# Kernel optimization log

Measured on AMD Instinct MI355X. Metric: run time of the kernel, lower is better.

## Reference

```python
import jax, jax.numpy as jnp
import numpy as np

N_NODES = 50000
N_EDGES = 1000000
N_QUERY = 100000
NUM_FEATURES = 256
HIDDEN = 256
LABEL_DIM = 2


def glorot(key, shape):
    lim = float(np.sqrt(6.0 / (shape[0] + shape[1])))
    return jax.random.uniform(key, shape, jnp.float32, -lim, lim)


def setup_inputs() -> dict:
    key = jax.random.key(0)
    ks = jax.random.split(key, 8)
    x = jax.random.normal(ks[0], (N_NODES, NUM_FEATURES), jnp.float32)
    edge_index = jax.random.randint(ks[1], (2, N_EDGES), 0, N_NODES)
    query_edges = jax.random.randint(ks[2], (N_QUERY, 2), 0, N_NODES)
    edge_weight = jax.random.uniform(ks[3], (N_EDGES,), jnp.float32)
    W1 = glorot(ks[4], (NUM_FEATURES, HIDDEN))
    b1 = jnp.zeros((HIDDEN,), jnp.float32)
    W2 = glorot(ks[5], (HIDDEN, HIDDEN))
    b2 = jnp.zeros((HIDDEN,), jnp.float32)
    Wl = glorot(ks[6], (2 * HIDDEN, LABEL_DIM))
    bl = jnp.zeros((LABEL_DIM,), jnp.float32)
    return {"x": x, "edge_index": edge_index, "query_edges": query_edges,
            "edge_weight": edge_weight, "W1": W1, "b1": b1, "W2": W2,
            "b2": b2, "Wl": Wl, "bl": bl}


def digcn_conv(x, edge_index, edge_weight, W, b):
    # x: [N, F_in] -> h: [N, F_out]; propagate: out[dst] += w_e * h[src]
    h = x @ W
    src, dst = edge_index[0], edge_index[1]
    msg = h[src] * edge_weight[:, None]            # [E, F_out]
    agg = jax.ops.segment_sum(msg, dst, num_segments=x.shape[0])
    return agg + b


def reference(x, edge_index, query_edges, edge_weight, W1, b1, W2, b2, Wl, bl):
    h = jax.nn.relu(digcn_conv(x, edge_index, edge_weight, W1, b1))
    # dropout is identity at eval time
    h = digcn_conv(h, edge_index, edge_weight, W2, b2)
    q = jnp.concatenate((h[query_edges[:, 0]], h[query_edges[:, 1]]), axis=-1)
    logits = q @ Wl + bl
    return jax.nn.log_softmax(logits, axis=1)
```

## Files before the change

kernel.cpp:

```cpp
#include <hip/hip_runtime.h>
#include <hip/hip_bf16.h>
#include <math.h>

typedef __bf16 bf16;
typedef __bf16 v8bf __attribute__((ext_vector_type(8)));
typedef __bf16 v4bf __attribute__((ext_vector_type(4)));
typedef float  v4f  __attribute__((ext_vector_type(4)));

#define FDIM 256
#define BKT_CAP 8192
#define AROW 264
#define P3CAP 4096


__global__ __launch_bounds__(256) void flag_kernel(float* __restrict__ out, int n) {
  int i = blockIdx.x * 256 + threadIdx.x;
  if (i < n) out[i] = 1.0e9f;
}

__global__ __launch_bounds__(256) void k1_prep(const float* __restrict__ W1,
                                               const float* __restrict__ W2,
                                               bf16* __restrict__ Wt1,
                                               const int* __restrict__ dst,
                                               int* __restrict__ phist,
                                               const float* __restrict__ Wl,
                                               const float* __restrict__ b2,
                                               const float* __restrict__ bl,
                                               float4* __restrict__ V,
                                               float* __restrict__ cc,
                                               int E, int N, int nbkt) {
  __shared__ int h[256];
  __shared__ float sWl[1024];
  __shared__ float red[256];
  int b = blockIdx.x;
  int t = threadIdx.x;
  if (b < 256) {
    int k = b;
    Wt1[t * FDIM + k] = (bf16)W1[k * FDIM + t];
  } else if (b < 512) {
    int pb = b - 256;
    int chunk = (E + 255) >> 8;
    int lo = pb * chunk;
    int hi = lo + chunk; if (hi > E) hi = E;
    h[t] = 0;
    __syncthreads();
    for (int e = lo + t; e < hi; e += 256) {
      int d = dst[e];
      d = d < 0 ? 0 : (d >= N ? N - 1 : d);
      atomicAdd(&h[d >> 8], 1);
    }
    __syncthreads();
    phist[pb * 256 + t] = h[t];
  } else {
#pragma unroll
    for (int j = 0; j < 4; ++j) sWl[j * 256 + t] = Wl[j * 256 + t];
    __syncthreads();
    const float* w2row = W2 + (size_t)t * FDIM;
    float4 acc = make_float4(0.f, 0.f, 0.f, 0.f);
    for (int j = 0; j < 256; ++j) {
      float w = w2row[j];
      acc.x += w * sWl[2 * j + 0];
      acc.y += w * sWl[2 * j + 1];
      acc.z += w * sWl[512 + 2 * j + 0];
      acc.w += w * sWl[512 + 2 * j + 1];
    }
    V[t] = acc;
    float bj = b2[t];
    red[t] = bj * (sWl[2 * t + 0] + sWl[512 + 2 * t + 0]);
    __syncthreads();
    if (t == 0) {
      float s = 0.f;
      for (int j = 0; j < 256; ++j) s += red[j];
      cc[0] = s + bl[0];
    }
    __syncthreads();
    red[t] = bj * (sWl[2 * t + 1] + sWl[512 + 2 * t + 1]);
    __syncthreads();
    if (t == 0) {
      float s = 0.f;
      for (int j = 0; j < 256; ++j) s += red[j];
      cc[1] = s + bl[1];
    }
  }
}

__global__ __launch_bounds__(256) void p2_scan(const int* __restrict__ phist,
                                               int* __restrict__ bbase,
                                               int* __restrict__ pbase,
                                               int* __restrict__ offs,
                                               int nbkt, int Nn) {
  __shared__ int wsum[4];
  int t = threadIdx.x, lane = t & 63, wv = t >> 6;
  int v = 0;
  for (int pb = 0; pb < 256; ++pb) v += phist[pb * 256 + t];
  if (t >= nbkt) v = 0;
  int x = v;
#pragma unroll
  for (int d = 1; d < 64; d <<= 1) {
    int y = __shfl_up(x, d, 64);
    if (lane >= d) x += y;
  }
  if (lane == 63) wsum[wv] = x;
  __syncthreads();
  int woff = 0;
  if (wv >= 1) woff += wsum[0];
  if (wv >= 2) woff += wsum[1];
  if (wv >= 3) woff += wsum[2];
  int incl = woff + x;
  int excl = incl - v;
  if (t < nbkt) bbase[t] = excl;
  if (t == 255) {
    bbase[nbkt] = incl;
    offs[Nn] = incl;
  }
  int run = excl;
#pragma unroll 4
  for (int pb = 0; pb < 256; ++pb) {
    pbase[pb * 256 + t] = run;
    run += phist[pb * 256 + t];
  }
}

__device__ inline void stage64(const float* __restrict__ A, bf16* __restrict__ As,
                               int row0, int M, int tid) {
#pragma unroll
  for (int j = 0; j < 8; ++j) {
    int g = j * 2048 + tid * 8;
    int r = g >> 8, c = g & 255;
    int gr = row0 + r; if (gr >= M) gr = M - 1;
    const float* p = A + (size_t)gr * FDIM + c;
    float4 f0 = *reinterpret_cast<const float4*>(p);
    float4 f1 = *reinterpret_cast<const float4*>(p + 4);
    v8bf o;
    o[0] = (bf16)f0.x; o[1] = (bf16)f0.y; o[2] = (bf16)f0.z; o[3] = (bf16)f0.w;
    o[4] = (bf16)f1.x; o[5] = (bf16)f1.y; o[6] = (bf16)f1.z; o[7] = (bf16)f1.w;
    *reinterpret_cast<v8bf*>(As + r * AROW + c) = o;
  }
}

__global__ __launch_bounds__(256, 2) void gemm1(const float* __restrict__ A,
                                                const bf16* __restrict__ Bt,
                                                bf16* __restrict__ C, int M) {
  __shared__ bf16 As[64 * AROW];
  const int K = FDIM, N = FDIM;
  int tid = threadIdx.x;
  int wave = tid >> 6;
  int lane = tid & 63;
  int l15 = lane & 15, quad = lane >> 4;

  v8bf bfr[4][8];
#pragma unroll
  for (int nn = 0; nn < 4; ++nn) {
    const bf16* bp = Bt + (size_t)(wave * 64 + nn * 16 + l15) * K + quad * 8;
#pragma unroll
    for (int kk = 0; kk < 8; ++kk)
      bfr[nn][kk] = *reinterpret_cast<const v8bf*>(bp + kk * 32);
  }

  int ntiles = (M + 63) >> 6;
  for (int tile = blockIdx.x; tile < ntiles; tile += gridDim.x) {
    int row0 = tile * 64;
    __syncthreads();
    stage64(A, As, row0, M, tid);
    __syncthreads();

#pragma unroll
    for (int st = 0; st < 4; ++st) {
      v8bf afr[8];
#pragma unroll
      for (int kk = 0; kk < 8; ++kk)
        afr[kk] = *reinterpret_cast<const v8bf*>(As + (st * 16 + l15) * AROW + quad * 8 + kk * 32);

      v4f acc[4];
#pragma unroll
      for (int nn = 0; nn < 4; ++nn) acc[nn] = (v4f){0.f, 0.f, 0.f, 0.f};

#pragma unroll
      for (int kk = 0; kk < 8; ++kk)
#pragma unroll
        for (int nn = 0; nn < 4; ++nn)
          acc[nn] = __builtin_amdgcn_mfma_f32_16x16x32_bf16(afr[kk], bfr[nn][kk], acc[nn], 0, 0, 0);

#pragma unroll
      for (int nn = 0; nn < 4; ++nn)
#pragma unroll
        for (int r = 0; r < 4; ++r) {
          int row = row0 + st * 16 + quad * 4 + r;
          int col = wave * 64 + nn * 16 + l15;
          if (row < M) C[(size_t)row * N + col] = (bf16)acc[nn][r];
        }
    }
  }
}

__global__ __launch_bounds__(256) void p3_scatter(const int* __restrict__ src,
                                                  const int* __restrict__ dst,
                                                  const float* __restrict__ ew,
                                                  const int* __restrict__ phist,
                                                  const int* __restrict__ pbase,
                                                  uint2* __restrict__ tmp,
                                                  int E, int N) {
  __shared__ uint2 ent[P3CAP];
  __shared__ int lbase[256];
  __shared__ int lcnt[256];
  __shared__ int gbase[256];
  __shared__ int wsum[4];
  int pb = blockIdx.x, t = threadIdx.x, lane = t & 63, wv = t >> 6;
  int chunk = (E + 255) >> 8;
  int lo = pb * chunk;
  int hi = lo + chunk; if (hi > E) hi = E;

  int v = phist[pb * 256 + t];
  int x = v;
#pragma unroll
  for (int d = 1; d < 64; d <<= 1) {
    int y = __shfl_up(x, d, 64);
    if (lane >= d) x += y;
  }
  if (lane == 63) wsum[wv] = x;
  gbase[t] = pbase[pb * 256 + t];
  lcnt[t] = 0;
  __syncthreads();
  int woff = 0;
  if (wv >= 1) woff += wsum[0];
  if (wv >= 2) woff += wsum[1];
  if (wv >= 3) woff += wsum[2];
  lbase[t] = woff + x - v;
  __syncthreads();

  for (int e = lo + t; e < hi; e += 256) {
    int d = dst[e];
    d = d < 0 ? 0 : (d >= N ? N - 1 : d);
    int b = d >> 8;
    int sv = src[e];
    sv = sv < 0 ? 0 : (sv >= N ? N - 1 : sv);
    unsigned int u = __float_as_uint(ew[e]);
    unsigned int wbits = ((u + 0x7FFFu + ((u >> 16) & 1u)) & 0xFFFF0000u);
    unsigned int meta = wbits | (unsigned int)(sv & 0xFFFF);
    int r = atomicAdd(&lcnt[b], 1);
    int pos = lbase[b] + r;
    if (pos >= 0 && pos < P3CAP) ent[pos] = make_uint2(meta, (unsigned int)d);
  }
  __syncthreads();

  int count = hi - lo;
  for (int i = t; i < count; i += 256) {
    uint2 en = ent[i];
    int b = (int)(en.y >> 8);
    int dest = gbase[b] + (i - lbase[b]);
    if (dest >= 0 && dest < E) tmp[dest] = en;
  }
}

__global__ __launch_bounds__(256, 1) void p4_sort(const uint2* __restrict__ tmp,
                                                  const int* __restrict__ bbase,
                                                  unsigned int* __restrict__ pmeta,
                                                  int* __restrict__ offs,
                                                  int Nn, int E) {
  __shared__ uint2 ent[BKT_CAP];
  __shared__ unsigned int outm[BKT_CAP];
  __shared__ int h2[256], ex2[256], c2[256];
  __shared__ int wsum[4];
  int b = blockIdx.x, t = threadIdx.x, lane = t & 63, wv = t >> 6;
  int s0 = bbase[b], s1 = bbase[b + 1];
  int count = s1 - s0;
  if (count < 0) count = 0;
  if (count > BKT_CAP) count = BKT_CAP;
  for (int i = t; i < count; i += 256) ent[i] = tmp[s0 + i];
  h2[t] = 0; c2[t] = 0;
  __syncthreads();
  for (int i = t; i < count; i += 256) atomicAdd(&h2[ent[i].y & 255u], 1);
  __syncthreads();
  int v = h2[t];
  int x = v;
#pragma unroll
  for (int d = 1; d < 64; d <<= 1) {
    int y = __shfl_up(x, d, 64);
    if (lane >= d) x += y;
  }
  if (lane == 63) wsum[wv] = x;
  __syncthreads();
  int woff = 0;
  if (wv >= 1) woff += wsum[0];
  if (wv >= 2) woff += wsum[1];
  if (wv >= 3) woff += wsum[2];
  int excl = woff + x - v;
  ex2[t] = excl;
  int node = (b << 8) + t;
  if (node < Nn) offs[node] = s0 + excl;
  __syncthreads();
  for (int i = t; i < count; i += 256) {
    int l = (int)(ent[i].y & 255u);
    int r = atomicAdd(&c2[l], 1);
    outm[ex2[l] + r] = ent[i].x;
  }
  __syncthreads();
  for (int i = t; i < count; i += 256) pmeta[s0 + i] = outm[i];
}

__global__ __launch_bounds__(256) void agg1G(const bf16* __restrict__ T,
                                             const unsigned int* __restrict__ pmeta,
                                             const int* __restrict__ offsets,
                                             const float* __restrict__ bias,
                                             const float4* __restrict__ V,
                                             float4* __restrict__ G,
                                             int node_lo, int node_hi, int E, int N) {
  int wid = blockIdx.x * 4 + (threadIdx.x >> 6);
  int nw = gridDim.x * 4;
  int lane = threadIdx.x & 63;
  int f = lane * 4;
  const bf16* Tf = T + f;

  float4 bb = *reinterpret_cast<const float4*>(bias + f);
  float4 v0 = V[f + 0], v1 = V[f + 1], v2 = V[f + 2], v3 = V[f + 3];

  for (int node = node_lo + wid; node < node_hi; node += nw) {
    int nb = __builtin_amdgcn_readfirstlane(node);
    int beg = offsets[nb], end = offsets[nb + 1];
    beg = beg < 0 ? 0 : (beg > E ? E : beg);
    end = end < beg ? beg : (end > E ? E : end);
    int cnt = end - beg;
    const unsigned int* m = pmeta + beg;

    float a0 = 0.f, a1 = 0.f, a2 = 0.f, a3 = 0.f;
    int p = 0;
    for (; p + 8 <= cnt; p += 8) {
      unsigned int mv0 = m[p + 0], mv1 = m[p + 1], mv2 = m[p + 2], mv3 = m[p + 3];
      unsigned int mv4 = m[p + 4], mv5 = m[p + 5], mv6 = m[p + 6], mv7 = m[p + 7];
      v4bf t0 = *reinterpret_cast<const v4bf*>(Tf + ((size_t)(mv0 & 0xFFFFu) << 8));
      v4bf t1 = *reinterpret_cast<const v4bf*>(Tf + ((size_t)(mv1 & 0xFFFFu) << 8));
      v4bf t2 = *reinterpret_cast<const v4bf*>(Tf + ((size_t)(mv2 & 0xFFFFu) << 8));
      v4bf t3 = *reinterpret_cast<const v4bf*>(Tf + ((size_t)(mv3 & 0xFFFFu) << 8));
      v4bf t4 = *reinterpret_cast<const v4bf*>(Tf + ((size_t)(mv4 & 0xFFFFu) << 8));
      v4bf t5 = *reinterpret_cast<const v4bf*>(Tf + ((size_t)(mv5 & 0xFFFFu) << 8));
      v4bf t6 = *reinterpret_cast<const v4bf*>(Tf + ((size_t)(mv6 & 0xFFFFu) << 8));
      v4bf t7 = *reinterpret_cast<const v4bf*>(Tf + ((size_t)(mv7 & 0xFFFFu) << 8));
      float w0 = __uint_as_float(mv0 & 0xFFFF0000u);
      float w1 = __uint_as_float(mv1 & 0xFFFF0000u);
      float w2 = __uint_as_float(mv2 & 0xFFFF0000u);
      float w3 = __uint_as_float(mv3 & 0xFFFF0000u);
      float w4 = __uint_as_float(mv4 & 0xFFFF0000u);
      float w5 = __uint_as_float(mv5 & 0xFFFF0000u);
      float w6 = __uint_as_float(mv6 & 0xFFFF0000u);
      float w7 = __uint_as_float(mv7 & 0xFFFF0000u);
      a0 += w0 * (float)t0[0]; a1 += w0 * (float)t0[1]; a2 += w0 * (float)t0[2]; a3 += w0 * (float)t0[3];
      a0 += w1 * (float)t1[0]; a1 += w1 * (float)t1[1]; a2 += w1 * (float)t1[2]; a3 += w1 * (float)t1[3];
      a0 += w2 * (float)t2[0]; a1 += w2 * (float)t2[1]; a2 += w2 * (float)t2[2]; a3 += w2 * (float)t2[3];
      a0 += w3 * (float)t3[0]; a1 += w3 * (float)t3[1]; a2 += w3 * (float)t3[2]; a3 += w3 * (float)t3[3];
      a0 += w4 * (float)t4[0]; a1 += w4 * (float)t4[1]; a2 += w4 * (float)t4[2]; a3 += w4 * (float)t4[3];
      a0 += w5 * (float)t5[0]; a1 += w5 * (float)t5[1]; a2 += w5 * (float)t5[2]; a3 += w5 * (float)t5[3];
      a0 += w6 * (float)t6[0]; a1 += w6 * (float)t6[1]; a2 += w6 * (float)t6[2]; a3 += w6 * (float)t6[3];
      a0 += w7 * (float)t7[0]; a1 += w7 * (float)t7[1]; a2 += w7 * (float)t7[2]; a3 += w7 * (float)t7[3];
    }
    for (; p < cnt; ++p) {
      unsigned int mv = m[p];
      float w = __uint_as_float(mv & 0xFFFF0000u);
      v4bf tv = *reinterpret_cast<const v4bf*>(Tf + ((size_t)(mv & 0xFFFFu) << 8));
      a0 += w * (float)tv[0];
      a1 += w * (float)tv[1];
      a2 += w * (float)tv[2];
      a3 += w * (float)tv[3];
    }

    float r0 = fmaxf(a0 + bb.x, 0.f);
    float r1 = fmaxf(a1 + bb.y, 0.f);
    float r2 = fmaxf(a2 + bb.z, 0.f);
    float r3 = fmaxf(a3 + bb.w, 0.f);

    float gx = r0 * v0.x + r1 * v1.x + r2 * v2.x + r3 * v3.x;
    float gy = r0 * v0.y + r1 * v1.y + r2 * v2.y + r3 * v3.y;
    float gz = r0 * v0.z + r1 * v1.z + r2 * v2.z + r3 * v3.z;
    float gw = r0 * v0.w + r1 * v1.w + r2 * v2.w + r3 * v3.w;
#pragma unroll
    for (int d = 32; d > 0; d >>= 1) {
      gx += __shfl_down(gx, d, 64);
      gy += __shfl_down(gy, d, 64);
      gz += __shfl_down(gz, d, 64);
      gw += __shfl_down(gw, d, 64);
    }
    if (lane == 0) G[node] = make_float4(gx, gy, gz, gw);
  }
}

__global__ __launch_bounds__(256) void aggP(const float4* __restrict__ G,
                                            const unsigned int* __restrict__ pmeta,
                                            const int* __restrict__ offsets,
                                            float4* __restrict__ P, int N, int E) {
  int node = blockIdx.x * 64 + (threadIdx.x >> 2);
  if (node >= N) return;
  int j = threadIdx.x & 3;
  int beg = offsets[node], end = offsets[node + 1];
  beg = beg < 0 ? 0 : (beg > E ? E : beg);
  end = end < beg ? beg : (end > E ? E : end);
  float ax = 0.f, ay = 0.f, az = 0.f, aw = 0.f;
  int p = beg + j;
  for (; p + 4 < end; p += 8) {
    unsigned int m0 = pmeta[p], m1 = pmeta[p + 4];
    int s0 = (int)(m0 & 0xFFFFu); s0 = s0 >= N ? N - 1 : s0;
    int s1 = (int)(m1 & 0xFFFFu); s1 = s1 >= N ? N - 1 : s1;
    float4 g0 = G[s0], g1 = G[s1];
    float w0 = __uint_as_float(m0 & 0xFFFF0000u);
    float w1 = __uint_as_float(m1 & 0xFFFF0000u);
    ax += w0 * g0.x + w1 * g1.x;
    ay += w0 * g0.y + w1 * g1.y;
    az += w0 * g0.z + w1 * g1.z;
    aw += w0 * g0.w + w1 * g1.w;
  }
  if (p < end) {
    unsigned int mm = pmeta[p];
    int s = (int)(mm & 0xFFFFu); s = s >= N ? N - 1 : s;
    float w = __uint_as_float(mm & 0xFFFF0000u);
    float4 g = G[s];
    ax += w * g.x; ay += w * g.y; az += w * g.z; aw += w * g.w;
  }
  ax += __shfl_xor(ax, 1, 64); ax += __shfl_xor(ax, 2, 64);
  ay += __shfl_xor(ay, 1, 64); ay += __shfl_xor(ay, 2, 64);
  az += __shfl_xor(az, 1, 64); az += __shfl_xor(az, 2, 64);
  aw += __shfl_xor(aw, 1, 64); aw += __shfl_xor(aw, 2, 64);
  if (j == 0) P[node] = make_float4(ax, ay, az, aw);
}

__global__ __launch_bounds__(256) void query_small(const int* __restrict__ qe,
                                                   const float4* __restrict__ P,
                                                   const float* __restrict__ cc,
                                                   float* __restrict__ out, int Q, int N) {
  int q = blockIdx.x * 256 + threadIdx.x;
  if (q >= Q) return;
  int n0 = qe[2 * q + 0]; n0 = n0 < 0 ? 0 : (n0 >= N ? N - 1 : n0);
  int n1 = qe[2 * q + 1]; n1 = n1 < 0 ? 0 : (n1 >= N ? N - 1 : n1);
  float4 p0 = P[n0];
  float4 p1 = P[n1];
  float l0 = p0.x + p1.z + cc[0];
  float l1 = p0.y + p1.w + cc[1];
  float m = fmaxf(l0, l1);
  float lse = m + logf(expf(l0 - m) + expf(l1 - m));
  out[2 * q + 0] = l0 - lse;
  out[2 * q + 1] = l1 - lse;
}


extern "C" void kernel_launch(void* const* d_in, const int* in_sizes, int n_in,
                              void* d_out, int out_size, void* d_ws, size_t ws_size,
                              hipStream_t stream) {
  const float* x  = (const float*)d_in[0];
  const int*   ei = (const int*)d_in[1];
  const int*   qe = (const int*)d_in[2];
  const float* ew = (const float*)d_in[3];
  const float* W1 = (const float*)d_in[4];
  const float* b1 = (const float*)d_in[5];
  const float* W2 = (const float*)d_in[6];
  const float* b2 = (const float*)d_in[7];
  const float* Wl = (const float*)d_in[8];
  const float* bl = (const float*)d_in[9];

  int N = in_sizes[0] / FDIM;
  int E = in_sizes[1] / 2;
  int Q = in_sizes[2] / 2;
  const int* srcv = ei;
  const int* dstv = ei + E;
  int nbkt = (N + 255) >> 8;
  int ntiles = (N + 63) >> 6;

  size_t off = 0;
  auto alloc = [&](size_t bytes) -> void* {
    void* p = (char*)d_ws + off;
    off += (bytes + 255) & ~(size_t)255;
    return p;
  };
  bf16* bufT  = (bf16*)alloc((size_t)N * FDIM * 2);
  uint2* tmp  = (uint2*)alloc((size_t)E * 8);
  bf16* Wt1   = (bf16*)alloc((size_t)FDIM * FDIM * 2);
  int* offs   = (int*)alloc((size_t)(N + 1) * 4);
  unsigned int* pmeta = (unsigned int*)alloc((size_t)E * 4);
  float4* G   = (float4*)alloc((size_t)N * 16);
  float4* P   = (float4*)alloc((size_t)N * 16);
  float4* V   = (float4*)alloc(256 * 16);
  float* cc   = (float*)alloc(2 * 4);
  int* phist  = (int*)alloc(256 * 256 * 4);
  int* pbase  = (int*)alloc(256 * 256 * 4);
  int* bbase  = (int*)alloc(257 * 4);

  if (off > ws_size) {
    flag_kernel<<<(out_size + 255) / 256, 256, 0, stream>>>((float*)d_out, out_size);
    return;
  }

  k1_prep<<<513, 256, 0, stream>>>(W1, W2, Wt1, dstv, phist, Wl, b2, bl, V, cc,
                                   E, N, nbkt);
  p2_scan<<<1, 256, 0, stream>>>(phist, bbase, pbase, offs, nbkt, N);
  gemm1<<<ntiles, 256, 0, stream>>>(x, Wt1, bufT, N);
  p3_scatter<<<256, 256, 0, stream>>>(srcv, dstv, ew, phist, pbase, tmp, E, N);
  p4_sort<<<nbkt, 256, 0, stream>>>(tmp, bbase, pmeta, offs, N, E);

  int q1 = N >> 2, q2 = N >> 1, q3 = q1 + q2;
  agg1G<<<2048, 256, 0, stream>>>(bufT, pmeta, offs, b1, V, G, 0, q1, E, N);
  agg1G<<<2048, 256, 0, stream>>>(bufT, pmeta, offs, b1, V, G, q1, q2, E, N);
  agg1G<<<2048, 256, 0, stream>>>(bufT, pmeta, offs, b1, V, G, q2, q3, E, N);
  agg1G<<<2048, 256, 0, stream>>>(bufT, pmeta, offs, b1, V, G, q3, N, E, N);

  aggP<<<(N * 4 + 255) / 256, 256, 0, stream>>>(G, pmeta, offs, P, N, E);

  query_small<<<(Q + 255) / 256, 256, 0, stream>>>(qe, P, cc, (float*)d_out, Q, N);
}
```

Baseline: 279.5 us.

## Fold global bucket scan into scatter/sort kernels and merge agg1G launches

Removes the single-block p2_scan kernel by having each p3_scatter and p4_sort block recompute the column-sum and prefix scan of the partition histogram redundantly. It also replaces four quarter-range agg1G launches with one launch over all nodes. The goal is fewer kernel launches and less serialization on a tiny one-block kernel. The cost is that every block now reads the full 256x256 histogram, which adds redundant global loads.

```diff
diff --git a/kernel.cpp b/kernel.cpp
--- a/kernel.cpp
+++ b/kernel.cpp
@@ -84,43 +84,6 @@
   }
 }
 
-__global__ __launch_bounds__(256) void p2_scan(const int* __restrict__ phist,
-                                               int* __restrict__ bbase,
-                                               int* __restrict__ pbase,
-                                               int* __restrict__ offs,
-                                               int nbkt, int Nn) {
-  __shared__ int wsum[4];
-  int t = threadIdx.x, lane = t & 63, wv = t >> 6;
-  int v = 0;
-  for (int pb = 0; pb < 256; ++pb) v += phist[pb * 256 + t];
-  if (t >= nbkt) v = 0;
-  int x = v;
-#pragma unroll
-  for (int d = 1; d < 64; d <<= 1) {
-    int y = __shfl_up(x, d, 64);
-    if (lane >= d) x += y;
-  }
-  if (lane == 63) wsum[wv] = x;
-  __syncthreads();
-  int woff = 0;
-  if (wv >= 1) woff += wsum[0];
-  if (wv >= 2) woff += wsum[1];
-  if (wv >= 3) woff += wsum[2];
-  int incl = woff + x;
-  int excl = incl - v;
-  if (t < nbkt) bbase[t] = excl;
-  if (t == 255) {
-    bbase[nbkt] = incl;
-    offs[Nn] = incl;
-  }
-  int run = excl;
-#pragma unroll 4
-  for (int pb = 0; pb < 256; ++pb) {
-    pbase[pb * 256 + t] = run;
-    run += phist[pb * 256 + t];
-  }
-}
-
 __device__ inline void stage64(const float* __restrict__ A, bf16* __restrict__ As,
                                int row0, int M, int tid) {
 #pragma unroll
@@ -197,7 +160,6 @@
                                                   const int* __restrict__ dst,
                                                   const float* __restrict__ ew,
                                                   const int* __restrict__ phist,
-                                                  const int* __restrict__ pbase,
                                                   uint2* __restrict__ tmp,
                                                   int E, int N) {
   __shared__ uint2 ent[P3CAP];
@@ -210,22 +172,40 @@
   int lo = pb * chunk;
   int hi = lo + chunk; if (hi > E) hi = E;
 
-  int v = phist[pb * 256 + t];
-  int x = v;
+  int tot = 0, pref = 0, mine = 0;
+  for (int c = 0; c < 256; ++c) {
+    int v = phist[c * 256 + t];
+    if (c == pb) { pref = tot; mine = v; }
+    tot += v;
+  }
+  int x = tot;
 #pragma unroll
   for (int d = 1; d < 64; d <<= 1) {
     int y = __shfl_up(x, d, 64);
     if (lane >= d) x += y;
   }
   if (lane == 63) wsum[wv] = x;
-  gbase[t] = pbase[pb * 256 + t];
   lcnt[t] = 0;
   __syncthreads();
   int woff = 0;
   if (wv >= 1) woff += wsum[0];
   if (wv >= 2) woff += wsum[1];
   if (wv >= 3) woff += wsum[2];
-  lbase[t] = woff + x - v;
+  gbase[t] = (woff + x - tot) + pref;
+  __syncthreads();
+  int x2 = mine;
+#pragma unroll
+  for (int d = 1; d < 64; d <<= 1) {
+    int y = __shfl_up(x2, d, 64);
+    if (lane >= d) x2 += y;
+  }
+  if (lane == 63) wsum[wv] = x2;
+  __syncthreads();
+  int woff2 = 0;
+  if (wv >= 1) woff2 += wsum[0];
+  if (wv >= 2) woff2 += wsum[1];
+  if (wv >= 3) woff2 += wsum[2];
+  lbase[t] = woff2 + x2 - mine;
   __syncthreads();
 
   for (int e = lo + t; e < hi; e += 256) {
@@ -253,38 +233,60 @@
 }
 
 __global__ __launch_bounds__(256, 1) void p4_sort(const uint2* __restrict__ tmp,
-                                                  const int* __restrict__ bbase,
+                                                  const int* __restrict__ phist,
                                                   unsigned int* __restrict__ pmeta,
                                                   int* __restrict__ offs,
                                                   int Nn, int E) {
   __shared__ uint2 ent[BKT_CAP];
   __shared__ unsigned int outm[BKT_CAP];
   __shared__ int h2[256], ex2[256], c2[256];
+  __shared__ int exb[256], totb[256];
   __shared__ int wsum[4];
   int b = blockIdx.x, t = threadIdx.x, lane = t & 63, wv = t >> 6;
-  int s0 = bbase[b], s1 = bbase[b + 1];
+
+  int tot = 0;
+  for (int c = 0; c < 256; ++c) tot += phist[c * 256 + t];
+  int x = tot;
+#pragma unroll
+  for (int d = 1; d < 64; d <<= 1) {
+    int y = __shfl_up(x, d, 64);
+    if (lane >= d) x += y;
+  }
+  if (lane == 63) wsum[wv] = x;
+  h2[t] = 0; c2[t] = 0;
+  __syncthreads();
+  int woff = 0;
+  if (wv >= 1) woff += wsum[0];
+  if (wv >= 2) woff += wsum[1];
+  if (wv >= 3) woff += wsum[2];
+  exb[t] = woff + x - tot;
+  totb[t] = tot;
+  __syncthreads();
+  int s0 = exb[b];
+  int s1 = s0 + totb[b];
+  if (b == 0 && t == 0) offs[Nn] = exb[255] + totb[255];
+
   int count = s1 - s0;
   if (count < 0) count = 0;
   if (count > BKT_CAP) count = BKT_CAP;
   for (int i = t; i < count; i += 256) ent[i] = tmp[s0 + i];
-  h2[t] = 0; c2[t] = 0;
   __syncthreads();
   for (int i = t; i < count; i += 256) atomicAdd(&h2[ent[i].y & 255u], 1);
   __syncthreads();
   int v = h2[t];
-  int x = v;
+  int x2 = v;
 #pragma unroll
   for (int d = 1; d < 64; d <<= 1) {
-    int y = __shfl_up(x, d, 64);
-    if (lane >= d) x += y;
-  }
-  if (lane == 63) wsum[wv] = x;
-  __syncthreads();
-  int woff = 0;
-  if (wv >= 1) woff += wsum[0];
-  if (wv >= 2) woff += wsum[1];
-  if (wv >= 3) woff += wsum[2];
-  int excl = woff + x - v;
+    int y = __shfl_up(x2, d, 64);
+    if (lane >= d) x2 += y;
+  }
+  if (lane == 63) wsum[wv] = x2;
+  __syncthreads();
+  int woff2 = 0;
+  if (wv >= 1) woff2 += wsum[0];
+  if (wv >= 2) woff2 += wsum[1];
+  if (wv >= 3) woff2 += wsum[2];
+  int excl = woff2 + x2 - v;
   ex2[t] = excl;
   int node = (b << 8) + t;
   if (node < Nn) offs[node] = s0 + excl;
@@ -303,8 +305,7 @@
                                              const int* __restrict__ offsets,
                                              const float* __restrict__ bias,
                                              const float4* __restrict__ V,
-                                             float4* __restrict__ G,
-                                             int node_lo, int node_hi, int E, int N) {
+                                             float4* __restrict__ G, int N, int E) {
   int wid = blockIdx.x * 4 + (threadIdx.x >> 6);
   int nw = gridDim.x * 4;
   int lane = threadIdx.x & 63;
@@ -314,7 +315,7 @@
   float4 bb = *reinterpret_cast<const float4*>(bias + f);
   float4 v0 = V[f + 0], v1 = V[f + 1], v2 = V[f + 2], v3 = V[f + 3];
 
-  for (int node = node_lo + wid; node < node_hi; node += nw) {
+  for (int node = wid; node < N; node += nw) {
     int nb = __builtin_amdgcn_readfirstlane(node);
     int beg = offsets[nb], end = offsets[nb + 1];
     beg = beg < 0 ? 0 : (beg > E ? E : beg);
@@ -477,8 +478,6 @@
   float4* V   = (float4*)alloc(256 * 16);
   float* cc   = (float*)alloc(2 * 4);
   int* phist  = (int*)alloc(256 * 256 * 4);
-  int* pbase  = (int*)alloc(256 * 256 * 4);
-  int* bbase  = (int*)alloc(257 * 4);
 
   if (off > ws_size) {
     flag_kernel<<<(out_size + 255) / 256, 256, 0, stream>>>((float*)d_out, out_size);
@@ -487,16 +486,11 @@
 
   k1_prep<<<513, 256, 0, stream>>>(W1, W2, Wt1, dstv, phist, Wl, b2, bl, V, cc,
                                    E, N, nbkt);
-  p2_scan<<<1, 256, 0, stream>>>(phist, bbase, pbase, offs, nbkt, N);
   gemm1<<<ntiles, 256, 0, stream>>>(x, Wt1, bufT, N);
-  p3_scatter<<<256, 256, 0, stream>>>(srcv, dstv, ew, phist, pbase, tmp, E, N);
-  p4_sort<<<nbkt, 256, 0, stream>>>(tmp, bbase, pmeta, offs, N, E);
-
-  int q1 = N >> 2, q2 = N >> 1, q3 = q1 + q2;
-  agg1G<<<2048, 256, 0, stream>>>(bufT, pmeta, offs, b1, V, G, 0, q1, E, N);
-  agg1G<<<2048, 256, 0, stream>>>(bufT, pmeta, offs, b1, V, G, q1, q2, E, N);
-  agg1G<<<2048, 256, 0, stream>>>(bufT, pmeta, offs, b1, V, G, q2, q3, E, N);
-  agg1G<<<2048, 256, 0, stream>>>(bufT, pmeta, offs, b1, V, G, q3, N, E, N);
+  p3_scatter<<<256, 256, 0, stream>>>(srcv, dstv, ew, phist, tmp, E, N);
+  p4_sort<<<nbkt, 256, 0, stream>>>(tmp, phist, pmeta, offs, N, E);
+
+  agg1G<<<2048, 256, 0, stream>>>(bufT, pmeta, offs, b1, V, G, N, E);
 
   aggP<<<(N * 4 + 255) / 256, 256, 0, stream>>>(G, pmeta, offs, P, N, E);
 
```

Result: faster. 261.9 us (-6.3%).

## Fuse pipeline stages into two cooperative persistent kernels with grid syncs

Applied to the files above, without the earlier changes.

Collapses the chain of small launches (prep, scan, GEMM, scatter, sort, four aggregation passes, projection, query) into two cooperative kernels that separate phases with grid.sync(), removing launch overhead and inter-kernel gaps. The p4 sort now writes to global memory directly instead of staging through a shared output buffer, which lowers its shared memory use. The fallback path also merges the four split aggregation launches into one. In exchange, megaA runs with a fixed grid of 512 blocks, so the GEMM and sort get fewer blocks than before and are limited by the shared-memory occupancy of the fused kernel. If the cooperative launch fails, the code falls back to separate launches.

```diff
diff --git a/kernel.cpp b/kernel.cpp
--- a/kernel.cpp
+++ b/kernel.cpp
@@ -1,6 +1,9 @@
 #include <hip/hip_runtime.h>
+#include <hip/hip_cooperative_groups.h>
 #include <hip/hip_bf16.h>
 #include <math.h>
+
+namespace cg = cooperative_groups;
 
 typedef __bf16 bf16;
 typedef __bf16 v8bf __attribute__((ext_vector_type(8)));
@@ -11,6 +14,7 @@
 #define BKT_CAP 8192
 #define AROW 264
 #define P3CAP 4096
+#define SMEM_A 68640
 
 
 __global__ __launch_bounds__(256) void flag_kernel(float* __restrict__ out, int n) {
@@ -18,27 +22,21 @@
   if (i < n) out[i] = 1.0e9f;
 }
 
-__global__ __launch_bounds__(256) void k1_prep(const float* __restrict__ W1,
-                                               const float* __restrict__ W2,
-                                               bf16* __restrict__ Wt1,
-                                               const int* __restrict__ dst,
-                                               int* __restrict__ phist,
-                                               const float* __restrict__ Wl,
-                                               const float* __restrict__ b2,
-                                               const float* __restrict__ bl,
-                                               float4* __restrict__ V,
-                                               float* __restrict__ cc,
-                                               int E, int N, int nbkt) {
-  __shared__ int h[256];
-  __shared__ float sWl[1024];
-  __shared__ float red[256];
-  int b = blockIdx.x;
+
+__device__ void k1_body(int vb, char* sm, const float* __restrict__ W1,
+                        const float* __restrict__ W2, bf16* __restrict__ Wt1,
+                        const int* __restrict__ dst, int* __restrict__ phist,
+                        const float* __restrict__ Wl, const float* __restrict__ b2,
+                        const float* __restrict__ bl, float4* __restrict__ V,
+                        float* __restrict__ cc, int E, int N) {
+  int* h = (int*)sm;
+  float* sWl = (float*)(sm + 1024);
+  float* red = (float*)(sm + 5120);
   int t = threadIdx.x;
-  if (b < 256) {
-    int k = b;
-    Wt1[t * FDIM + k] = (bf16)W1[k * FDIM + t];
-  } else if (b < 512) {
-    int pb = b - 256;
+  if (vb < 256) {
+    Wt1[t * FDIM + vb] = (bf16)W1[vb * FDIM + t];
+  } else if (vb < 512) {
+    int pb = vb - 256;
     int chunk = (E + 255) >> 8;
     int lo = pb * chunk;
     int hi = lo + chunk; if (hi > E) hi = E;
@@ -51,6 +49,7 @@
     }
     __syncthreads();
     phist[pb * 256 + t] = h[t];
+    __syncthreads();
   } else {
 #pragma unroll
     for (int j = 0; j < 4; ++j) sWl[j * 256 + t] = Wl[j * 256 + t];
@@ -81,15 +80,14 @@
       for (int j = 0; j < 256; ++j) s += red[j];
       cc[1] = s + bl[1];
     }
-  }
-}
-
-__global__ __launch_bounds__(256) void p2_scan(const int* __restrict__ phist,
-                                               int* __restrict__ bbase,
-                                               int* __restrict__ pbase,
-                                               int* __restrict__ offs,
-                                               int nbkt, int Nn) {
-  __shared__ int wsum[4];
+    __syncthreads();
+  }
+}
+
+__device__ void p2_body(char* sm, const int* __restrict__ phist,
+                        int* __restrict__ bbase, int* __restrict__ pbase,
+                        int* __restrict__ offs, int nbkt, int Nn) {
+  int* wsum = (int*)sm;
   int t = threadIdx.x, lane = t & 63, wv = t >> 6;
   int v = 0;
   for (int pb = 0; pb < 256; ++pb) v += phist[pb * 256 + t];
@@ -121,8 +119,8 @@
   }
 }
 
-__device__ inline void stage64(const float* __restrict__ A, bf16* __restrict__ As,
-                               int row0, int M, int tid) {
+__device__ void stage64(const float* __restrict__ A, bf16* __restrict__ As,
+                        int row0, int M, int tid) {
 #pragma unroll
   for (int j = 0; j < 8; ++j) {
     int g = j * 2048 + tid * 8;
@@ -138,10 +136,9 @@
   }
 }
 
-__global__ __launch_bounds__(256, 2) void gemm1(const float* __restrict__ A,
-                                                const bf16* __restrict__ Bt,
-                                                bf16* __restrict__ C, int M) {
-  __shared__ bf16 As[64 * AROW];
+__device__ void gemm_body(const float* __restrict__ A, const bf16* __restrict__ Bt,
+                          bf16* __restrict__ C, int M, int bid, int nblocks,
+                          bf16* As) {
   const int K = FDIM, N = FDIM;
   int tid = threadIdx.x;
   int wave = tid >> 6;
@@ -158,7 +155,7 @@
   }
 
   int ntiles = (M + 63) >> 6;
-  for (int tile = blockIdx.x; tile < ntiles; tile += gridDim.x) {
+  for (int tile = bid; tile < ntiles; tile += nblocks) {
     int row0 = tile * 64;
     __syncthreads();
     stage64(A, As, row0, M, tid);
@@ -193,19 +190,16 @@
   }
 }
 
-__global__ __launch_bounds__(256) void p3_scatter(const int* __restrict__ src,
-                                                  const int* __restrict__ dst,
-                                                  const float* __restrict__ ew,
-                                                  const int* __restrict__ phist,
-                                                  const int* __restrict__ pbase,
-                                                  uint2* __restrict__ tmp,
-                                                  int E, int N) {
-  __shared__ uint2 ent[P3CAP];
-  __shared__ int lbase[256];
-  __shared__ int lcnt[256];
-  __shared__ int gbase[256];
-  __shared__ int wsum[4];
-  int pb = blockIdx.x, t = threadIdx.x, lane = t & 63, wv = t >> 6;
+__device__ void p3_body(int pb, char* sm, const int* __restrict__ src,
+                        const int* __restrict__ dst, const float* __restrict__ ew,
+                        const int* __restrict__ phist, const int* __restrict__ pbase,
+                        uint2* __restrict__ tmp, int E, int N) {
+  uint2* ent = (uint2*)sm;
+  int* lbase = (int*)(sm + 32768);
+  int* lcnt  = (int*)(sm + 33792);
+  int* gbase = (int*)(sm + 34816);
+  int* wsum  = (int*)(sm + 35840);
+  int t = threadIdx.x, lane = t & 63, wv = t >> 6;
   int chunk = (E + 255) >> 8;
   int lo = pb * chunk;
   int hi = lo + chunk; if (hi > E) hi = E;
@@ -250,18 +244,18 @@
     int dest = gbase[b] + (i - lbase[b]);
     if (dest >= 0 && dest < E) tmp[dest] = en;
   }
-}
-
-__global__ __launch_bounds__(256, 1) void p4_sort(const uint2* __restrict__ tmp,
-                                                  const int* __restrict__ bbase,
-                                                  unsigned int* __restrict__ pmeta,
-                                                  int* __restrict__ offs,
-                                                  int Nn, int E) {
-  __shared__ uint2 ent[BKT_CAP];
-  __shared__ unsigned int outm[BKT_CAP];
-  __shared__ int h2[256], ex2[256], c2[256];
-  __shared__ int wsum[4];
-  int b = blockIdx.x, t = threadIdx.x, lane = t & 63, wv = t >> 6;
+  __syncthreads();
+}
+
+__device__ void p4_body(int b, char* sm, const uint2* __restrict__ tmp,
+                        const int* __restrict__ bbase, unsigned int* __restrict__ pmeta,
+                        int* __restrict__ offs, int Nn, int E) {
+  uint2* ent = (uint2*)sm;
+  int* h2  = (int*)(sm + 65536);
+  int* ex2 = (int*)(sm + 66560);
+  int* c2  = (int*)(sm + 67584);
+  int* wsum = (int*)(sm + 68608);
+  int t = threadIdx.x, lane = t & 63, wv = t >> 6;
   int s0 = bbase[b], s1 = bbase[b + 1];
   int count = s1 - s0;
   if (count < 0) count = 0;
@@ -292,19 +286,16 @@
   for (int i = t; i < count; i += 256) {
     int l = (int)(ent[i].y & 255u);
     int r = atomicAdd(&c2[l], 1);
-    outm[ex2[l] + r] = ent[i].x;
-  }
-  __syncthreads();
-  for (int i = t; i < count; i += 256) pmeta[s0 + i] = outm[i];
-}
-
-__global__ __launch_bounds__(256) void agg1G(const bf16* __restrict__ T,
-                                             const unsigned int* __restrict__ pmeta,
-                                             const int* __restrict__ offsets,
-                                             const float* __restrict__ bias,
-                                             const float4* __restrict__ V,
-                                             float4* __restrict__ G,
-                                             int node_lo, int node_hi, int E, int N) {
+    int pos = s0 + ex2[l] + r;
+    if (pos >= 0 && pos < E) pmeta[pos] = ent[i].x;
+  }
+  __syncthreads();
+}
+
+__device__ void agg_body(const bf16* __restrict__ T, const unsigned int* __restrict__ pmeta,
+                         const int* __restrict__ offsets, const float* __restrict__ bias,
+                         const float4* __restrict__ V, float4* __restrict__ G,
+                         int N, int E) {
   int wid = blockIdx.x * 4 + (threadIdx.x >> 6);
   int nw = gridDim.x * 4;
   int lane = threadIdx.x & 63;
@@ -314,7 +305,7 @@
   float4 bb = *reinterpret_cast<const float4*>(bias + f);
   float4 v0 = V[f + 0], v1 = V[f + 1], v2 = V[f + 2], v3 = V[f + 3];
 
-  for (int node = node_lo + wid; node < node_hi; node += nw) {
+  for (int node = wid; node < N; node += nw) {
     int nb = __builtin_amdgcn_readfirstlane(node);
     int beg = offsets[nb], end = offsets[nb + 1];
     beg = beg < 0 ? 0 : (beg > E ? E : beg);
@@ -382,60 +373,162 @@
   }
 }
 
+__device__ void aggP_body(const float4* __restrict__ G, const unsigned int* __restrict__ pmeta,
+                          const int* __restrict__ offsets, float4* __restrict__ P,
+                          int N, int E) {
+  int nvb = (N + 63) >> 6;
+  int j = threadIdx.x & 3;
+  for (int vb = blockIdx.x; vb < nvb; vb += gridDim.x) {
+    int node = vb * 64 + (threadIdx.x >> 2);
+    if (node < N) {
+      int beg = offsets[node], end = offsets[node + 1];
+      beg = beg < 0 ? 0 : (beg > E ? E : beg);
+      end = end < beg ? beg : (end > E ? E : end);
+      float ax = 0.f, ay = 0.f, az = 0.f, aw = 0.f;
+      int p = beg + j;
+      for (; p + 4 < end; p += 8) {
+        unsigned int m0 = pmeta[p], m1 = pmeta[p + 4];
+        int s0 = (int)(m0 & 0xFFFFu); s0 = s0 >= N ? N - 1 : s0;
+        int s1 = (int)(m1 & 0xFFFFu); s1 = s1 >= N ? N - 1 : s1;
+        float4 g0 = G[s0], g1 = G[s1];
+        float w0 = __uint_as_float(m0 & 0xFFFF0000u);
+        float w1 = __uint_as_float(m1 & 0xFFFF0000u);
+        ax += w0 * g0.x + w1 * g1.x;
+        ay += w0 * g0.y + w1 * g1.y;
+        az += w0 * g0.z + w1 * g1.z;
+        aw += w0 * g0.w + w1 * g1.w;
+      }
+      if (p < end) {
+        unsigned int mm = pmeta[p];
+        int s = (int)(mm & 0xFFFFu); s = s >= N ? N - 1 : s;
+        float w = __uint_as_float(mm & 0xFFFF0000u);
+        float4 g = G[s];
+        ax += w * g.x; ay += w * g.y; az += w * g.z; aw += w * g.w;
+      }
+      ax += __shfl_xor(ax, 1, 64); ax += __shfl_xor(ax, 2, 64);
+      ay += __shfl_xor(ay, 1, 64); ay += __shfl_xor(ay, 2, 64);
+      az += __shfl_xor(az, 1, 64); az += __shfl_xor(az, 2, 64);
+      aw += __shfl_xor(aw, 1, 64); aw += __shfl_xor(aw, 2, 64);
+      if (j == 0) P[node] = make_float4(ax, ay, az, aw);
+    }
+  }
+}
+
+__device__ void query_body(const int* __restrict__ qe, const float4* __restrict__ P,
+                           const float* __restrict__ cc, float* __restrict__ out,
+                           int Q, int N) {
+  int nvb = (Q + 255) >> 8;
+  for (int vb = blockIdx.x; vb < nvb; vb += gridDim.x) {
+    int q = vb * 256 + threadIdx.x;
+    if (q < Q) {
+      int n0 = qe[2 * q + 0]; n0 = n0 < 0 ? 0 : (n0 >= N ? N - 1 : n0);
+      int n1 = qe[2 * q + 1]; n1 = n1 < 0 ? 0 : (n1 >= N ? N - 1 : n1);
+      float4 p0 = P[n0];
+      float4 p1 = P[n1];
+      float l0 = p0.x + p1.z + cc[0];
+      float l1 = p0.y + p1.w + cc[1];
+      float m = fmaxf(l0, l1);
+      float lse = m + logf(expf(l0 - m) + expf(l1 - m));
+      out[2 * q + 0] = l0 - lse;
+      out[2 * q + 1] = l1 - lse;
+    }
+  }
+}
+
+
+__global__ __launch_bounds__(256, 2) void megaA(const float* __restrict__ W1,
+    const float* __restrict__ W2, bf16* __restrict__ Wt1, const int* __restrict__ dst,
+    int* __restrict__ phist, const float* __restrict__ Wl, const float* __restrict__ b2,
+    const float* __restrict__ bl, float4* __restrict__ V, float* __restrict__ cc,
+    int* __restrict__ bbase, int* __restrict__ pbase, int* __restrict__ offs,
+    const float* __restrict__ x, bf16* __restrict__ bufT, const int* __restrict__ src,
+    const float* __restrict__ ew, uint2* __restrict__ tmp,
+    unsigned int* __restrict__ pmeta, int E, int N, int nbkt) {
+  cg::grid_group grid = cg::this_grid();
+  __shared__ __align__(16) char sm[SMEM_A];
+
+  for (int vb = blockIdx.x; vb < 513; vb += gridDim.x)
+    k1_body(vb, sm, W1, W2, Wt1, dst, phist, Wl, b2, bl, V, cc, E, N);
+  grid.sync();
+  if (blockIdx.x == 0) p2_body(sm, phist, bbase, pbase, offs, nbkt, N);
+  grid.sync();
+  gemm_body(x, Wt1, bufT, N, blockIdx.x, gridDim.x, (bf16*)sm);
+  grid.sync();
+  for (int vb = blockIdx.x; vb < 256; vb += gridDim.x)
+    p3_body(vb, sm, src, dst, ew, phist, pbase, tmp, E, N);
+  grid.sync();
+  for (int vb = blockIdx.x; vb < nbkt; vb += gridDim.x)
+    p4_body(vb, sm, tmp, bbase, pmeta, offs, N, E);
+}
+
+__global__ __launch_bounds__(256, 8) void megaB(const bf16* __restrict__ bufT,
+    const unsigned int* __restrict__ pmeta, const int* __restrict__ offs,
+    const float* __restrict__ b1, const float4* __restrict__ V, float4* __restrict__ G,
+    float4* __restrict__ P, const int* __restrict__ qe, const float* __restrict__ cc,
+    float* __restrict__ out, int N, int E, int Q) {
+  cg::grid_group grid = cg::this_grid();
+  agg_body(bufT, pmeta, offs, b1, V, G, N, E);
+  grid.sync();
+  aggP_body(G, pmeta, offs, P, N, E);
+  grid.sync();
+  query_body(qe, P, cc, out, Q, N);
+}
+
+
+__global__ __launch_bounds__(256) void k1_prep(const float* __restrict__ W1,
+    const float* __restrict__ W2, bf16* __restrict__ Wt1, const int* __restrict__ dst,
+    int* __restrict__ phist, const float* __restrict__ Wl, const float* __restrict__ b2,
+    const float* __restrict__ bl, float4* __restrict__ V, float* __restrict__ cc,
+    int E, int N) {
+  __shared__ __align__(16) char sm[6144];
+  k1_body(blockIdx.x, sm, W1, W2, Wt1, dst, phist, Wl, b2, bl, V, cc, E, N);
+}
+
+__global__ __launch_bounds__(256) void p2_scan(const int* __restrict__ phist,
+    int* __restrict__ bbase, int* __restrict__ pbase, int* __restrict__ offs,
+    int nbkt, int Nn) {
+  __shared__ __align__(16) char sm[16];
+  p2_body(sm, phist, bbase, pbase, offs, nbkt, Nn);
+}
+
+__global__ __launch_bounds__(256, 2) void gemm1(const float* __restrict__ A,
+    const bf16* __restrict__ Bt, bf16* __restrict__ C, int M) {
+  __shared__ __align__(16) char sm[64 * AROW * 2];
+  gemm_body(A, Bt, C, M, blockIdx.x, gridDim.x, (bf16*)sm);
+}
+
+__global__ __launch_bounds__(256) void p3_scatter(const int* __restrict__ src,
+    const int* __restrict__ dst, const float* __restrict__ ew,
+    const int* __restrict__ phist, const int* __restrict__ pbase,
+    uint2* __restrict__ tmp, int E, int N) {
+  __shared__ __align__(16) char sm[35856];
+  p3_body(blockIdx.x, sm, src, dst, ew, phist, pbase, tmp, E, N);
+}
+
+__global__ __launch_bounds__(256) void p4_sort(const uint2* __restrict__ tmp,
+    const int* __restrict__ bbase, unsigned int* __restrict__ pmeta,
+    int* __restrict__ offs, int Nn, int E) {
+  __shared__ __align__(16) char sm[SMEM_A];
+  p4_body(blockIdx.x, sm, tmp, bbase, pmeta, offs, Nn, E);
+}
+
+__global__ __launch_bounds__(256) void agg1G(const bf16* __restrict__ T,
+    const unsigned int* __restrict__ pmeta, const int* __restrict__ offsets,
+    const float* __restrict__ bias, const float4* __restrict__ V,
+    float4* __restrict__ G, int N, int E) {
+  agg_body(T, pmeta, offsets, bias, V, G, N, E);
+}
+
 __global__ __launch_bounds__(256) void aggP(const float4* __restrict__ G,
-                                            const unsigned int* __restrict__ pmeta,
-                                            const int* __restrict__ offsets,
-                                            float4* __restrict__ P, int N, int E) {
-  int node = blockIdx.x * 64 + (threadIdx.x >> 2);
-  if (node >= N) return;
-  int j = threadIdx.x & 3;
-  int beg = offsets[node], end = offsets[node + 1];
-  beg = beg < 0 ? 0 : (beg > E ? E : beg);
-  end = end < beg ? beg : (end > E ? E : end);
-  float ax = 0.f, ay = 0.f, az = 0.f, aw = 0.f;
-  int p = beg + j;
-  for (; p + 4 < end; p += 8) {
-    unsigned int m0 = pmeta[p], m1 = pmeta[p + 4];
-    int s0 = (int)(m0 & 0xFFFFu); s0 = s0 >= N ? N - 1 : s0;
-    int s1 = (int)(m1 & 0xFFFFu); s1 = s1 >= N ? N - 1 : s1;
-    float4 g0 = G[s0], g1 = G[s1];
-    float w0 = __uint_as_float(m0 & 0xFFFF0000u);
-    float w1 = __uint_as_float(m1 & 0xFFFF0000u);
-    ax += w0 * g0.x + w1 * g1.x;
-    ay += w0 * g0.y + w1 * g1.y;
-    az += w0 * g0.z + w1 * g1.z;
-    aw += w0 * g0.w + w1 * g1.w;
-  }
-  if (p < end) {
-    unsigned int mm = pmeta[p];
-    int s = (int)(mm & 0xFFFFu); s = s >= N ? N - 1 : s;
-    float w = __uint_as_float(mm & 0xFFFF0000u);
-    float4 g = G[s];
-    ax += w * g.x; ay += w * g.y; az += w * g.z; aw += w * g.w;
-  }
-  ax += __shfl_xor(ax, 1, 64); ax += __shfl_xor(ax, 2, 64);
-  ay += __shfl_xor(ay, 1, 64); ay += __shfl_xor(ay, 2, 64);
-  az += __shfl_xor(az, 1, 64); az += __shfl_xor(az, 2, 64);
-  aw += __shfl_xor(aw, 1, 64); aw += __shfl_xor(aw, 2, 64);
-  if (j == 0) P[node] = make_float4(ax, ay, az, aw);
+    const unsigned int* __restrict__ pmeta, const int* __restrict__ offsets,
+    float4* __restrict__ P, int N, int E) {
+  aggP_body(G, pmeta, offsets, P, N, E);
 }
 
 __global__ __launch_bounds__(256) void query_small(const int* __restrict__ qe,
-                                                   const float4* __restrict__ P,
-                                                   const float* __restrict__ cc,
-                                                   float* __restrict__ out, int Q, int N) {
-  int q = blockIdx.x * 256 + threadIdx.x;
-  if (q >= Q) return;
-  int n0 = qe[2 * q + 0]; n0 = n0 < 0 ? 0 : (n0 >= N ? N - 1 : n0);
-  int n1 = qe[2 * q + 1]; n1 = n1 < 0 ? 0 : (n1 >= N ? N - 1 : n1);
-  float4 p0 = P[n0];
-  float4 p1 = P[n1];
-  float l0 = p0.x + p1.z + cc[0];
-  float l1 = p0.y + p1.w + cc[1];
-  float m = fmaxf(l0, l1);
-  float lse = m + logf(expf(l0 - m) + expf(l1 - m));
-  out[2 * q + 0] = l0 - lse;
-  out[2 * q + 1] = l1 - lse;
+    const float4* __restrict__ P, const float* __restrict__ cc,
+    float* __restrict__ out, int Q, int N) {
+  query_body(qe, P, cc, out, Q, N);
 }
 
 
@@ -460,6 +553,7 @@
   const int* dstv = ei + E;
   int nbkt = (N + 255) >> 8;
   int ntiles = (N + 63) >> 6;
+  float* outp = (float*)d_out;
 
   size_t off = 0;
   auto alloc = [&](size_t bytes) -> void* {
@@ -485,20 +579,38 @@
     return;
   }
 
-  k1_prep<<<513, 256, 0, stream>>>(W1, W2, Wt1, dstv, phist, Wl, b2, bl, V, cc,
-                                   E, N, nbkt);
-  p2_scan<<<1, 256, 0, stream>>>(phist, bbase, pbase, offs, nbkt, N);
-  gemm1<<<ntiles, 256, 0, stream>>>(x, Wt1, bufT, N);
-  p3_scatter<<<256, 256, 0, stream>>>(srcv, dstv, ew, phist, pbase, tmp, E, N);
-  p4_sort<<<nbkt, 256, 0, stream>>>(tmp, bbase, pmeta, offs, N, E);
-
-  int q1 = N >> 2, q2 = N >> 1, q3 = q1 + q2;
-  agg1G<<<2048, 256, 0, stream>>>(bufT, pmeta, offs, b1, V, G, 0, q1, E, N);
-  agg1G<<<2048, 256, 0, stream>>>(bufT, pmeta, offs, b1, V, G, q1, q2, E, N);
-  agg1G<<<2048, 256, 0, stream>>>(bufT, pmeta, offs, b1, V, G, q2, q3, E, N);
-  agg1G<<<2048, 256, 0, stream>>>(bufT, pmeta, offs, b1, V, G, q3, N, E, N);
-
-  aggP<<<(N * 4 + 255) / 256, 256, 0, stream>>>(G, pmeta, offs, P, N, E);
-
-  query_small<<<(Q + 255) / 256, 256, 0, stream>>>(qe, P, cc, (float*)d_out, Q, N);
-}
+  int dev = 0;
+  hipGetDevice(&dev);
+  int coop = 0;
+  hipDeviceGetAttribute(&coop, hipDeviceAttributeCooperativeLaunch, dev);
+
+  bool done = false;
+  if (coop) {
+    void* argsA[] = {(void*)&W1, (void*)&W2, (void*)&Wt1, (void*)&dstv, (void*)&phist,
+                     (void*)&Wl, (void*)&b2, (void*)&bl, (void*)&V, (void*)&cc,
+                     (void*)&bbase, (void*)&pbase, (void*)&offs, (void*)&x, (void*)&bufT,
+                     (void*)&srcv, (void*)&ew, (void*)&tmp, (void*)&pmeta,
+                     (void*)&E, (void*)&N, (void*)&nbkt};
+    void* argsB[] = {(void*)&bufT, (void*)&pmeta, (void*)&offs, (void*)&b1, (void*)&V,
+                     (void*)&G, (void*)&P, (void*)&qe, (void*)&cc, (void*)&outp,
+                     (void*)&N, (void*)&E, (void*)&Q};
+    hipError_t eA = hipLaunchCooperativeKernel((const void*)megaA, dim3(512), dim3(256),
+                                               argsA, 0, stream);
+    if (eA == hipSuccess) {
+      hipError_t eB = hipLaunchCooperativeKernel((const void*)megaB, dim3(2048), dim3(256),
+                                                 argsB, 0, stream);
+      done = (eB == hipSuccess);
+    }
+  }
+
+  if (!done) {
+    k1_prep<<<513, 256, 0, stream>>>(W1, W2, Wt1, dstv, phist, Wl, b2, bl, V, cc, E, N);
+    p2_scan<<<1, 256, 0, stream>>>(phist, bbase, pbase, offs, nbkt, N);
+    gemm1<<<ntiles, 256, 0, stream>>>(x, Wt1, bufT, N);
+    p3_scatter<<<256, 256, 0, stream>>>(srcv, dstv, ew, phist, pbase, tmp, E, N);
+    p4_sort<<<nbkt, 256, 0, stream>>>(tmp, bbase, pmeta, offs, N, E);
+    agg1G<<<2048, 256, 0, stream>>>(bufT, pmeta, offs, b1, V, G, N, E);
+    aggP<<<(N * 4 + 255) / 256, 256, 0, stream>>>(G, pmeta, offs, P, N, E);
+    query_small<<<(Q + 255) / 256, 256, 0, stream>>>(qe, P, cc, outp, Q, N);
+  }
+}
```

Result: slower. 1.016 ms (+263.6%).
